# Kernel tuning notes

Measured on AMD Instinct MI355X. Metric: run time of the kernel, lower is better.

Reference implementation:

```python
import jax, jax.numpy as jnp
import numpy as np

# FP4 (e2m1) representable magnitudes: {0, 0.5, 1, 1.5, 2, 3, 4, 6}
_FP4_GRID = np.array([0.0, 0.5, 1.0, 1.5, 2.0, 3.0, 4.0, 6.0], dtype=np.float32)
_FP4_MIDS = (_FP4_GRID[1:] + _FP4_GRID[:-1]) / 2.0  # decision boundaries


def quant_fp4(x):
    """Per-tensor symmetric quantize-dequantize to FP4 e2m1 grid."""
    grid = jnp.asarray(_FP4_GRID, dtype=x.dtype)
    mids = jnp.asarray(_FP4_MIDS, dtype=x.dtype)
    scale = jnp.maximum(jnp.max(jnp.abs(x)) / 6.0, jnp.asarray(1e-12, x.dtype))
    xs = jnp.abs(x) / scale
    idx = jnp.searchsorted(mids, xs)  # nearest-grid-point index
    return jnp.sign(x) * grid[idx] * scale


def fp4_linear(x, w, b):
    # fake-quantized matmul: dequant(FP4(x)) @ dequant(FP4(w)) + b
    return jnp.matmul(quant_fp4(x), quant_fp4(w)) + b


def setup_inputs() -> dict:
    key = jax.random.key(0)
    k1, k2, k3 = jax.random.split(key, 3)
    B, D_IN, D_H, D_OUT = 4096, 4096, 16384, 4096
    x = jax.random.normal(k1, (B, D_IN), dtype=jnp.float32)
    w1 = jax.random.normal(k2, (D_IN, D_H), dtype=jnp.float32)
    b1 = jnp.zeros((D_H,), dtype=jnp.float32)
    w2 = jax.random.normal(k3, (D_H, D_OUT), dtype=jnp.float32)
    b2 = jnp.zeros((D_OUT,), dtype=jnp.float32)
    return {"x": x, "w1": w1, "b1": b1, "w2": w2, "b2": b2}


def reference(x, w1, b1, w2, b2):
    h = jax.nn.relu(fp4_linear(x, w1, b1))
    return fp4_linear(h, w2, b2)
```

## Files before the change

kernel.cpp:

```cpp
#include <hip/hip_runtime.h>
#include <hip/hip_bf16.h>


typedef float f32x4 __attribute__((ext_vector_type(4)));
typedef int   i32x4 __attribute__((ext_vector_type(4)));
typedef int   i32x8 __attribute__((ext_vector_type(8)));

#define AS1 __attribute__((address_space(1)))
#define AS3 __attribute__((address_space(3)))

__device__ __forceinline__ void wg_barrier() {
    asm volatile("" ::: "memory");
    __builtin_amdgcn_s_barrier();
    asm volatile("" ::: "memory");
}

__device__ __forceinline__ float scale_from_amax_bits(unsigned bits) {
    return fmaxf(__uint_as_float(bits) / 6.0f, 1e-12f);
}

__device__ __forceinline__ unsigned q4(float v, float inv_scale) {
    float xs = fabsf(v) * inv_scale;
    unsigned idx = 0;
    idx += (xs > 0.25f);
    idx += (xs > 0.75f);
    idx += (xs > 1.25f);
    idx += (xs > 1.75f);
    idx += (xs > 2.5f);
    idx += (xs > 3.5f);
    idx += (xs > 5.0f);
    return idx | ((v < 0.0f) ? 8u : 0u);
}

__global__ void zero4_kernel(unsigned* p) {
    if (threadIdx.x < 4) p[threadIdx.x] = 0u;
}

__global__ void sentinel_kernel(float* out, long long n) {
    long long i = (long long)blockIdx.x * blockDim.x + threadIdx.x;
    long long stride = (long long)gridDim.x * blockDim.x;
    for (; i < n; i += stride) out[i] = 1e30f;
}

__global__ void absmax3_kernel(const float* __restrict__ in0, long long n0,
                               const float* __restrict__ in1, long long n1,
                               const float* __restrict__ in2, long long n2,
                               unsigned* __restrict__ out) {
    const float* in;
    long long n;
    unsigned* o;
    long long nb, b = blockIdx.x;
    if (b < 512)       { in = in0; n = n0; o = out + 0; b -= 0;    nb = 512;  }
    else if (b < 2560) { in = in1; n = n1; o = out + 1; b -= 512;  nb = 2048; }
    else               { in = in2; n = n2; o = out + 3; b -= 2560; nb = 2048; }

    long long i = (b * blockDim.x + threadIdx.x) * 4;
    long long stride = nb * blockDim.x * 4;
    float m = 0.0f;
    for (; i < n; i += stride) {
        float4 v = *(const float4*)&in[i];
        m = fmaxf(m, fmaxf(fmaxf(fabsf(v.x), fabsf(v.y)),
                           fmaxf(fabsf(v.z), fabsf(v.w))));
    }
    #pragma unroll
    for (int off = 32; off > 0; off >>= 1)
        m = fmaxf(m, __shfl_xor(m, off));
    __shared__ float smax[4];
    int lane = threadIdx.x & 63, w = threadIdx.x >> 6;
    if (lane == 0) smax[w] = m;
    __syncthreads();
    if (threadIdx.x == 0) {
        m = fmaxf(fmaxf(smax[0], smax[1]), fmaxf(smax[2], smax[3]));
        atomicMax(o, __float_as_uint(m));
    }
}

__global__ void quant_pack_kernel(const float* __restrict__ in, long long n,
                                  const unsigned* __restrict__ amax,
                                  unsigned* __restrict__ out) {
    float inv = 1.0f / scale_from_amax_bits(*amax);
    long long i = ((long long)blockIdx.x * blockDim.x + threadIdx.x) * 8;
    long long stride = (long long)gridDim.x * blockDim.x * 8;
    for (; i < n; i += stride) {
        float4 a = *(const float4*)&in[i];
        float4 b = *(const float4*)&in[i + 4];
        unsigned u = q4(a.x, inv)        | (q4(a.y, inv) << 4)
                   | (q4(a.z, inv) << 8) | (q4(a.w, inv) << 12)
                   | (q4(b.x, inv) << 16)| (q4(b.y, inv) << 20)
                   | (q4(b.z, inv) << 24)| (q4(b.w, inv) << 28);
        out[i >> 3] = u;
    }
}

__global__ void quant_transpose_pack_kernel(const float* __restrict__ in, int R, int C,
                                            const unsigned* __restrict__ amax,
                                            unsigned char* __restrict__ out) {
    __shared__ float tile[64][65];
    float inv = 1.0f / scale_from_amax_bits(*amax);
    int t = threadIdx.x;
    int CT = C >> 6;
    int tc = blockIdx.x % CT;
    int tr = blockIdx.x / CT;
    int r0 = t >> 4;
    int c0 = (t & 15) * 4;
    #pragma unroll
    for (int it = 0; it < 4; ++it) {
        int r = r0 + it * 16;
        float4 v = *(const float4*)&in[(size_t)(tr * 64 + r) * C + tc * 64 + c0];
        tile[r][c0 + 0] = v.x;
        tile[r][c0 + 1] = v.y;
        tile[r][c0 + 2] = v.z;
        tile[r][c0 + 3] = v.w;
    }
    __syncthreads();
    int c = t >> 2;
    int rch = (t & 3) * 16;
    unsigned u0 = 0, u1 = 0;
    #pragma unroll
    for (int j = 0; j < 8; ++j) u0 |= q4(tile[rch + j][c], inv) << (4 * j);
    #pragma unroll
    for (int j = 0; j < 8; ++j) u1 |= q4(tile[rch + 8 + j][c], inv) << (4 * j);
    uint2 o; o.x = u0; o.y = u1;
    *(uint2*)&out[(size_t)(tc * 64 + c) * (R >> 1) + (size_t)(tr * 32) + (rch >> 1)] = o;
}

__device__ __forceinline__ f32x4 mm16(i32x4 a, i32x4 b, f32x4 c) {
    i32x8 a8 = {a[0], a[1], a[2], a[3], 0, 0, 0, 0};
    i32x8 b8 = {b[0], b[1], b[2], b[3], 0, 0, 0, 0};
    return __builtin_amdgcn_mfma_scale_f32_16x16x128_f8f6f4(
        a8, b8, c, 4, 4,
        0, 0x7f7f7f7f,
        0, 0x7f7f7f7f);
}

template <int RELU, int FUSE_AMAX>
__global__ __launch_bounds__(256, 2)
void gemm_fp4_a(const unsigned char* __restrict__ Ap,
                const unsigned char* __restrict__ Bp,
                float* __restrict__ C, const float* __restrict__ bias,
                const unsigned* __restrict__ amaxA,
                const unsigned* __restrict__ amaxB,
                unsigned* __restrict__ amaxOut,
                int M, int N, int K) {
    __shared__ alignas(16) unsigned char As[2][128 * 128];
    __shared__ alignas(16) unsigned char Bs[2][128 * 128];
    __shared__ float smax[4];

    int nwg = gridDim.x, cpx = nwg >> 3;
    int wg = (blockIdx.x & 7) * cpx + (blockIdx.x >> 3);
    int MT = M >> 7;
    int tm = wg % MT, tn = wg / MT;

    int tid = threadIdx.x, lane = tid & 63, wid = tid >> 6;
    int wr = wid >> 1, wc = wid & 1;

    size_t Kb = (size_t)(K >> 1);

    int cs = ((lane & 7) ^ ((lane >> 3) & 7)) << 4;
    int srow = wid * 32 + (lane >> 3);
    const unsigned char* Abase = Ap + (size_t)(tm * 128 + srow) * Kb + cs;
    const unsigned char* Bbase = Bp + (size_t)(tn * 128 + srow) * Kb + cs;
    char* AsB = (char*)As;
    char* BsB = (char*)Bs;
    int ldsOff = wid * 4096;

#define STAGE_A(d, kt)                                                        \
    do {                                                                      \
        _Pragma("unroll")                                                     \
        for (int i_ = 0; i_ < 4; ++i_) {                                      \
            __builtin_amdgcn_global_load_lds(                                 \
                (const AS1 void*)(Abase + (size_t)(kt) * 128 +                \
                                  (size_t)(i_ * 8) * Kb),                     \
                (AS3 void*)(AsB + ((d) << 14) + ldsOff + i_ * 1024),          \
                16, 0, 0);                                                    \
            __builtin_amdgcn_global_load_lds(                                 \
                (const AS1 void*)(Bbase + (size_t)(kt) * 128 +                \
                                  (size_t)(i_ * 8) * Kb),                     \
                (AS3 void*)(BsB + ((d) << 14) + ldsOff + i_ * 1024),          \
                16, 0, 0);                                                    \
        }                                                                     \
    } while (0)

    f32x4 acc[4][4] = {};
    int rrA = wr * 64 + (lane & 15);
    int rrB = wc * 64 + (lane & 15);

    int KT = K >> 8;

    STAGE_A(0, 0);

    for (int t = 0; t < KT; ++t) {
        int d = t & 1;
        if (t + 1 < KT) {
            STAGE_A(d ^ 1, t + 1);
            __builtin_amdgcn_sched_barrier(0);
            asm volatile("s_waitcnt vmcnt(8)" ::: "memory");
        } else {
            asm volatile("s_waitcnt vmcnt(0)" ::: "memory");
        }
        wg_barrier();

        const char* Aq = AsB + (d << 14);
        const char* Bq = BsB + (d << 14);
        #pragma unroll
        for (int ks = 0; ks < 2; ++ks) {
            int slotOff = ((ks * 4 + (lane >> 4)) ^ (lane & 7)) << 4;
            i32x4 a[4], b[4];
            #pragma unroll
            for (int mi = 0; mi < 4; ++mi)
                a[mi] = *(const i32x4*)(Aq + (rrA + mi * 16) * 128 + slotOff);
            #pragma unroll
            for (int ni = 0; ni < 4; ++ni)
                b[ni] = *(const i32x4*)(Bq + (rrB + ni * 16) * 128 + slotOff);
            #pragma unroll
            for (int mi = 0; mi < 4; ++mi)
                #pragma unroll
                for (int ni = 0; ni < 4; ++ni)
                    acc[mi][ni] = mm16(a[mi], b[ni], acc[mi][ni]);
        }
        asm volatile("s_waitcnt lgkmcnt(0)" ::: "memory");
        wg_barrier();
    }
#undef STAGE_A

    float s = scale_from_amax_bits(*amaxA) * scale_from_amax_bits(*amaxB);
    float vmax = 0.0f;
    int rowBase = tm * 128 + wr * 64 + (lane >> 4) * 4;
    int colBase = tn * 128 + wc * 64 + (lane & 15);
    #pragma unroll
    for (int mi = 0; mi < 4; ++mi) {
        #pragma unroll
        for (int ni = 0; ni < 4; ++ni) {
            int col = colBase + ni * 16;
            float bv = bias[col];
            int row = rowBase + mi * 16;
            #pragma unroll
            for (int r = 0; r < 4; ++r) {
                float v = acc[mi][ni][r] * s + bv;
                if (RELU) v = fmaxf(v, 0.0f);
                if (FUSE_AMAX) vmax = fmaxf(vmax, fabsf(v));
                C[(size_t)(row + r) * N + col] = v;
            }
        }
    }
    if (FUSE_AMAX) {
        #pragma unroll
        for (int off = 32; off > 0; off >>= 1)
            vmax = fmaxf(vmax, __shfl_xor(vmax, off));
        if (lane == 0) smax[wid] = vmax;
        __syncthreads();
        if (tid == 0) {
            vmax = fmaxf(fmaxf(smax[0], smax[1]), fmaxf(smax[2], smax[3]));
            atomicMax(amaxOut, __float_as_uint(vmax));
        }
    }
}

template <int RELU, int FUSE_AMAX>
__global__ __launch_bounds__(256, 4)
void gemm_fp4_b(const unsigned char* __restrict__ Ap,
                const unsigned char* __restrict__ Bp,
                float* __restrict__ C, const float* __restrict__ bias,
                const unsigned* __restrict__ amaxA,
                const unsigned* __restrict__ amaxB,
                unsigned* __restrict__ amaxOut,
                int M, int N, int K) {
    __shared__ alignas(16) unsigned char As[2][128 * 64];
    __shared__ alignas(16) unsigned char Bs[2][128 * 64];
    __shared__ float smax[4];

    int nwg = gridDim.x, cpx = nwg >> 3;
    int wg = (blockIdx.x & 7) * cpx + (blockIdx.x >> 3);
    int MT = M >> 7;
    int tm = wg % MT, tn = wg / MT;

    int tid = threadIdx.x, lane = tid & 63, wid = tid >> 6;
    int wr = wid >> 1, wc = wid & 1;

    size_t Kb = (size_t)(K >> 1);

    int csw = ((tid & 3) ^ ((tid >> 3) & 3)) << 4;
    int srow = tid >> 2;
    const unsigned char* Abase = Ap + (size_t)(tm * 128 + srow) * Kb + csw;
    const unsigned char* Bbase = Bp + (size_t)(tn * 128 + srow) * Kb + csw;
    char* AsB = (char*)As;
    char* BsB = (char*)Bs;
    int dstOff = wid << 10;

#define STAGE_B(d, kt)                                                        \
    do {                                                                      \
        _Pragma("unroll")                                                     \
        for (int i_ = 0; i_ < 2; ++i_) {                                      \
            __builtin_amdgcn_global_load_lds(                                 \
                (const AS1 void*)(Abase + (size_t)(kt) * 64 +                 \
                                  (size_t)(i_ * 64) * Kb),                    \
                (AS3 void*)(AsB + ((d) << 13) + (i_ << 12) + dstOff),         \
                16, 0, 0);                                                    \
            __builtin_amdgcn_global_load_lds(                                 \
                (const AS1 void*)(Bbase + (size_t)(kt) * 64 +                 \
                                  (size_t)(i_ * 64) * Kb),                    \
                (AS3 void*)(BsB + ((d) << 13) + (i_ << 12) + dstOff),         \
                16, 0, 0);                                                    \
        }                                                                     \
    } while (0)

    f32x4 acc[4][4] = {};
    int rrA = wr * 64 + (lane & 15);
    int rrB = wc * 64 + (lane & 15);
    int slotOff = (((lane >> 4) ^ ((lane >> 1) & 3)) << 4);

    int KT = K >> 7;

    STAGE_B(0, 0);

    for (int t = 0; t < KT; ++t) {
        int d = t & 1;
        if (t + 1 < KT) {
            STAGE_B(d ^ 1, t + 1);
            __builtin_amdgcn_sched_barrier(0);
            asm volatile("s_waitcnt vmcnt(4)" ::: "memory");
        } else {
            asm volatile("s_waitcnt vmcnt(0)" ::: "memory");
        }
        wg_barrier();

        const char* Aq = AsB + (d << 13);
        const char* Bq = BsB + (d << 13);
        i32x4 a[4], b[4];
        #pragma unroll
        for (int mi = 0; mi < 4; ++mi)
            a[mi] = *(const i32x4*)(Aq + (rrA + mi * 16) * 64 + slotOff);
        #pragma unroll
        for (int ni = 0; ni < 4; ++ni)
            b[ni] = *(const i32x4*)(Bq + (rrB + ni * 16) * 64 + slotOff);
        #pragma unroll
        for (int mi = 0; mi < 4; ++mi)
            #pragma unroll
            for (int ni = 0; ni < 4; ++ni)
                acc[mi][ni] = mm16(a[mi], b[ni], acc[mi][ni]);

        asm volatile("s_waitcnt lgkmcnt(0)" ::: "memory");
        wg_barrier();
    }
#undef STAGE_B

    float s = scale_from_amax_bits(*amaxA) * scale_from_amax_bits(*amaxB);
    float vmax = 0.0f;
    int rowBase = tm * 128 + wr * 64 + (lane >> 4) * 4;
    int colBase = tn * 128 + wc * 64 + (lane & 15);
    #pragma unroll
    for (int mi = 0; mi < 4; ++mi) {
        #pragma unroll
        for (int ni = 0; ni < 4; ++ni) {
            int col = colBase + ni * 16;
            float bv = bias[col];
            int row = rowBase + mi * 16;
            #pragma unroll
            for (int r = 0; r < 4; ++r) {
                float v = acc[mi][ni][r] * s + bv;
                if (RELU) v = fmaxf(v, 0.0f);
                if (FUSE_AMAX) vmax = fmaxf(vmax, fabsf(v));
                C[(size_t)(row + r) * N + col] = v;
            }
        }
    }
    if (FUSE_AMAX) {
        #pragma unroll
        for (int off = 32; off > 0; off >>= 1)
            vmax = fmaxf(vmax, __shfl_xor(vmax, off));
        if (lane == 0) smax[wid] = vmax;
        __syncthreads();
        if (tid == 0) {
            vmax = fmaxf(fmaxf(smax[0], smax[1]), fmaxf(smax[2], smax[3]));
            atomicMax(amaxOut, __float_as_uint(vmax));
        }
    }
}

extern "C" void kernel_launch(void* const* d_in, const int* in_sizes, int n_in,
                              void* d_out, int out_size, void* d_ws, size_t ws_size,
                              hipStream_t stream) {
    const float* x  = (const float*)d_in[0];
    const float* w1 = (const float*)d_in[1];
    const float* b1 = (const float*)d_in[2];
    const float* w2 = (const float*)d_in[3];
    const float* b2 = (const float*)d_in[4];
    float* out = (float*)d_out;

    const int B = 4096, DIN = 4096, DH = 16384, DOUT = 4096;

    const size_t off_amax = 0;
    const size_t off_Xq   = 256;
    const size_t off_W    = off_Xq + (size_t)B * DIN / 2;
    const size_t off_h    = off_W + (size_t)DIN * DH / 2;
    const size_t off_Hq   = off_h + (size_t)B * DH * 4;
    const size_t needed   = off_Hq + (size_t)B * DH / 2;

    if (ws_size < needed) {
        sentinel_kernel<<<2048, 256, 0, stream>>>(out, (long long)out_size);
        return;
    }

    char* ws = (char*)d_ws;
    unsigned* amax = (unsigned*)(ws + off_amax);
    unsigned char* Xq = (unsigned char*)(ws + off_Xq);
    unsigned char* Wq = (unsigned char*)(ws + off_W);
    float*         h  = (float*)(ws + off_h);
    unsigned char* Hq = (unsigned char*)(ws + off_Hq);

    zero4_kernel<<<1, 64, 0, stream>>>(amax);

    absmax3_kernel<<<4608, 256, 0, stream>>>(x, (long long)B * DIN,
                                             w1, (long long)DIN * DH,
                                             w2, (long long)DH * DOUT, amax);

    quant_pack_kernel<<<2048, 256, 0, stream>>>(x, (long long)B * DIN, amax + 0,
                                                (unsigned*)Xq);
    quant_transpose_pack_kernel<<<(DIN / 64) * (DH / 64), 256, 0, stream>>>(
        w1, DIN, DH, amax + 1, Wq);

    gemm_fp4_a<1, 1><<<(B / 128) * (DH / 128), 256, 0, stream>>>(
        Xq, Wq, h, b1, amax + 0, amax + 1, amax + 2, B, DH, DIN);

    quant_pack_kernel<<<2048, 256, 0, stream>>>(h, (long long)B * DH, amax + 2,
                                                (unsigned*)Hq);
    quant_transpose_pack_kernel<<<(DH / 64) * (DOUT / 64), 256, 0, stream>>>(
        w2, DH, DOUT, amax + 3, Wq);

    gemm_fp4_b<0, 0><<<(B / 128) * (DOUT / 128), 256, 0, stream>>>(
        Hq, Wq, out, b2, amax + 2, amax + 3, nullptr, B, DOUT, DH);
}
```

Measured before the change: 733.4 us.

## Split absmax per tensor, reverse quant traversal for cache reuse, simplify GEMM pipelines

Result: faster. 709.7 us (-3.2%).

```diff
diff --git a/kernel.cpp b/kernel.cpp
--- a/kernel.cpp
+++ b/kernel.cpp
@@ -8,12 +8,6 @@
 
 #define AS1 __attribute__((address_space(1)))
 #define AS3 __attribute__((address_space(3)))
-
-__device__ __forceinline__ void wg_barrier() {
-    asm volatile("" ::: "memory");
-    __builtin_amdgcn_s_barrier();
-    asm volatile("" ::: "memory");
-}
 
 __device__ __forceinline__ float scale_from_amax_bits(unsigned bits) {
     return fmaxf(__uint_as_float(bits) / 6.0f, 1e-12f);
@@ -42,20 +36,10 @@
     for (; i < n; i += stride) out[i] = 1e30f;
 }
 
-__global__ void absmax3_kernel(const float* __restrict__ in0, long long n0,
-                               const float* __restrict__ in1, long long n1,
-                               const float* __restrict__ in2, long long n2,
-                               unsigned* __restrict__ out) {
-    const float* in;
-    long long n;
-    unsigned* o;
-    long long nb, b = blockIdx.x;
-    if (b < 512)       { in = in0; n = n0; o = out + 0; b -= 0;    nb = 512;  }
-    else if (b < 2560) { in = in1; n = n1; o = out + 1; b -= 512;  nb = 2048; }
-    else               { in = in2; n = n2; o = out + 3; b -= 2560; nb = 2048; }
-
-    long long i = (b * blockDim.x + threadIdx.x) * 4;
-    long long stride = nb * blockDim.x * 4;
+__global__ void absmax_kernel(const float* __restrict__ in, long long n,
+                              unsigned* __restrict__ out) {
+    long long i = ((long long)blockIdx.x * blockDim.x + threadIdx.x) * 4;
+    long long stride = (long long)gridDim.x * blockDim.x * 4;
     float m = 0.0f;
     for (; i < n; i += stride) {
         float4 v = *(const float4*)&in[i];
@@ -71,24 +55,26 @@
     __syncthreads();
     if (threadIdx.x == 0) {
         m = fmaxf(fmaxf(smax[0], smax[1]), fmaxf(smax[2], smax[3]));
-        atomicMax(o, __float_as_uint(m));
-    }
-}
-
-__global__ void quant_pack_kernel(const float* __restrict__ in, long long n,
-                                  const unsigned* __restrict__ amax,
-                                  unsigned* __restrict__ out) {
+        atomicMax(out, __float_as_uint(m));
+    }
+}
+
+__global__ void quant_pack_rev_kernel(const float* __restrict__ in, long long n,
+                                      const unsigned* __restrict__ amax,
+                                      unsigned* __restrict__ out) {
     float inv = 1.0f / scale_from_amax_bits(*amax);
-    long long i = ((long long)blockIdx.x * blockDim.x + threadIdx.x) * 8;
-    long long stride = (long long)gridDim.x * blockDim.x * 8;
-    for (; i < n; i += stride) {
+    long long nw = n >> 3;
+    long long gid = (long long)blockIdx.x * blockDim.x + threadIdx.x;
+    long long gs = (long long)gridDim.x * blockDim.x;
+    for (long long j = nw - 1 - gid; j >= 0; j -= gs) {
+        long long i = j * 8;
         float4 a = *(const float4*)&in[i];
         float4 b = *(const float4*)&in[i + 4];
         unsigned u = q4(a.x, inv)        | (q4(a.y, inv) << 4)
                    | (q4(a.z, inv) << 8) | (q4(a.w, inv) << 12)
                    | (q4(b.x, inv) << 16)| (q4(b.y, inv) << 20)
                    | (q4(b.z, inv) << 24)| (q4(b.w, inv) << 28);
-        out[i >> 3] = u;
+        out[j] = u;
     }
 }
 
@@ -98,9 +84,10 @@
     __shared__ float tile[64][65];
     float inv = 1.0f / scale_from_amax_bits(*amax);
     int t = threadIdx.x;
+    int bid = gridDim.x - 1 - blockIdx.x;
     int CT = C >> 6;
-    int tc = blockIdx.x % CT;
-    int tr = blockIdx.x / CT;
+    int tc = bid % CT;
+    int tr = bid / CT;
     int r0 = t >> 4;
     int c0 = (t & 15) * 4;
     #pragma unroll
@@ -128,22 +115,33 @@
     i32x8 a8 = {a[0], a[1], a[2], a[3], 0, 0, 0, 0};
     i32x8 b8 = {b[0], b[1], b[2], b[3], 0, 0, 0, 0};
     return __builtin_amdgcn_mfma_scale_f32_16x16x128_f8f6f4(
-        a8, b8, c, 4, 4,
-        0, 0x7f7f7f7f,
-        0, 0x7f7f7f7f);
-}
+        a8, b8, c, 4, 4, 0, 0x7f7f7f7f, 0, 0x7f7f7f7f);
+}
+
+#define AMAX_EPILOG                                                           \
+    if (FUSE_AMAX) {                                                          \
+        _Pragma("unroll")                                                     \
+        for (int off = 32; off > 0; off >>= 1)                                \
+            vmax = fmaxf(vmax, __shfl_xor(vmax, off));                        \
+        if (lane == 0) smax[wid] = vmax;                                      \
+        __syncthreads();                                                      \
+        if (tid == 0) {                                                       \
+            vmax = fmaxf(fmaxf(smax[0], smax[1]), fmaxf(smax[2], smax[3]));   \
+            atomicMax(amaxOut, __float_as_uint(vmax));                        \
+        }                                                                     \
+    }
 
 template <int RELU, int FUSE_AMAX>
 __global__ __launch_bounds__(256, 2)
-void gemm_fp4_a(const unsigned char* __restrict__ Ap,
-                const unsigned char* __restrict__ Bp,
-                float* __restrict__ C, const float* __restrict__ bias,
-                const unsigned* __restrict__ amaxA,
-                const unsigned* __restrict__ amaxB,
-                unsigned* __restrict__ amaxOut,
-                int M, int N, int K) {
-    __shared__ alignas(16) unsigned char As[2][128 * 128];
-    __shared__ alignas(16) unsigned char Bs[2][128 * 128];
+void gemm_fp4_g1(const unsigned char* __restrict__ Ap,
+                 const unsigned char* __restrict__ Bp,
+                 float* __restrict__ C, const float* __restrict__ bias,
+                 const unsigned* __restrict__ amaxA,
+                 const unsigned* __restrict__ amaxB,
+                 unsigned* __restrict__ amaxOut,
+                 int M, int N, int K) {
+    __shared__ alignas(16) unsigned char As[128 * 128];
+    __shared__ alignas(16) unsigned char Bs[128 * 128];
     __shared__ float smax[4];
 
     int nwg = gridDim.x, cpx = nwg >> 3;
@@ -164,64 +162,41 @@
     char* BsB = (char*)Bs;
     int ldsOff = wid * 4096;
 
-#define STAGE_A(d, kt)                                                        \
-    do {                                                                      \
-        _Pragma("unroll")                                                     \
-        for (int i_ = 0; i_ < 4; ++i_) {                                      \
-            __builtin_amdgcn_global_load_lds(                                 \
-                (const AS1 void*)(Abase + (size_t)(kt) * 128 +                \
-                                  (size_t)(i_ * 8) * Kb),                     \
-                (AS3 void*)(AsB + ((d) << 14) + ldsOff + i_ * 1024),          \
-                16, 0, 0);                                                    \
-            __builtin_amdgcn_global_load_lds(                                 \
-                (const AS1 void*)(Bbase + (size_t)(kt) * 128 +                \
-                                  (size_t)(i_ * 8) * Kb),                     \
-                (AS3 void*)(BsB + ((d) << 14) + ldsOff + i_ * 1024),          \
-                16, 0, 0);                                                    \
-        }                                                                     \
-    } while (0)
-
     f32x4 acc[4][4] = {};
     int rrA = wr * 64 + (lane & 15);
     int rrB = wc * 64 + (lane & 15);
 
     int KT = K >> 8;
-
-    STAGE_A(0, 0);
-
-    for (int t = 0; t < KT; ++t) {
-        int d = t & 1;
-        if (t + 1 < KT) {
-            STAGE_A(d ^ 1, t + 1);
-            __builtin_amdgcn_sched_barrier(0);
-            asm volatile("s_waitcnt vmcnt(8)" ::: "memory");
-        } else {
-            asm volatile("s_waitcnt vmcnt(0)" ::: "memory");
+    for (int kt = 0; kt < KT; ++kt) {
+        #pragma unroll
+        for (int i = 0; i < 4; ++i) {
+            __builtin_amdgcn_global_load_lds(
+                (const AS1 void*)(Abase + (size_t)kt * 128 + (size_t)(i * 8) * Kb),
+                (AS3 void*)(AsB + ldsOff + i * 1024), 16, 0, 0);
+            __builtin_amdgcn_global_load_lds(
+                (const AS1 void*)(Bbase + (size_t)kt * 128 + (size_t)(i * 8) * Kb),
+                (AS3 void*)(BsB + ldsOff + i * 1024), 16, 0, 0);
         }
-        wg_barrier();
-
-        const char* Aq = AsB + (d << 14);
-        const char* Bq = BsB + (d << 14);
+        __syncthreads();
+
         #pragma unroll
         for (int ks = 0; ks < 2; ++ks) {
             int slotOff = ((ks * 4 + (lane >> 4)) ^ (lane & 7)) << 4;
             i32x4 a[4], b[4];
             #pragma unroll
             for (int mi = 0; mi < 4; ++mi)
-                a[mi] = *(const i32x4*)(Aq + (rrA + mi * 16) * 128 + slotOff);
+                a[mi] = *(const i32x4*)(AsB + (rrA + mi * 16) * 128 + slotOff);
             #pragma unroll
             for (int ni = 0; ni < 4; ++ni)
-                b[ni] = *(const i32x4*)(Bq + (rrB + ni * 16) * 128 + slotOff);
+                b[ni] = *(const i32x4*)(BsB + (rrB + ni * 16) * 128 + slotOff);
             #pragma unroll
             for (int mi = 0; mi < 4; ++mi)
                 #pragma unroll
                 for (int ni = 0; ni < 4; ++ni)
                     acc[mi][ni] = mm16(a[mi], b[ni], acc[mi][ni]);
         }
-        asm volatile("s_waitcnt lgkmcnt(0)" ::: "memory");
-        wg_barrier();
-    }
-#undef STAGE_A
+        __syncthreads();
+    }
 
     float s = scale_from_amax_bits(*amaxA) * scale_from_amax_bits(*amaxB);
     float vmax = 0.0f;
@@ -243,28 +218,18 @@
             }
         }
     }
-    if (FUSE_AMAX) {
-        #pragma unroll
-        for (int off = 32; off > 0; off >>= 1)
-            vmax = fmaxf(vmax, __shfl_xor(vmax, off));
-        if (lane == 0) smax[wid] = vmax;
-        __syncthreads();
-        if (tid == 0) {
-            vmax = fmaxf(fmaxf(smax[0], smax[1]), fmaxf(smax[2], smax[3]));
-            atomicMax(amaxOut, __float_as_uint(vmax));
-        }
-    }
+    AMAX_EPILOG
 }
 
 template <int RELU, int FUSE_AMAX>
-__global__ __launch_bounds__(256, 4)
-void gemm_fp4_b(const unsigned char* __restrict__ Ap,
-                const unsigned char* __restrict__ Bp,
-                float* __restrict__ C, const float* __restrict__ bias,
-                const unsigned* __restrict__ amaxA,
-                const unsigned* __restrict__ amaxB,
-                unsigned* __restrict__ amaxOut,
-                int M, int N, int K) {
+__global__ __launch_bounds__(256, 2)
+void gemm_fp4_g2(const unsigned char* __restrict__ Ap,
+                 const unsigned char* __restrict__ Bp,
+                 float* __restrict__ C, const float* __restrict__ bias,
+                 const unsigned* __restrict__ amaxA,
+                 const unsigned* __restrict__ amaxB,
+                 unsigned* __restrict__ amaxOut,
+                 int M, int N, int K) {
     __shared__ alignas(16) unsigned char As[2][128 * 64];
     __shared__ alignas(16) unsigned char Bs[2][128 * 64];
     __shared__ float smax[4];
@@ -287,7 +252,7 @@
     char* BsB = (char*)Bs;
     int dstOff = wid << 10;
 
-#define STAGE_B(d, kt)                                                        \
+#define STAGE_G2(d, kt)                                                       \
     do {                                                                      \
         _Pragma("unroll")                                                     \
         for (int i_ = 0; i_ < 2; ++i_) {                                      \
@@ -310,19 +275,13 @@
     int slotOff = (((lane >> 4) ^ ((lane >> 1) & 3)) << 4);
 
     int KT = K >> 7;
-
-    STAGE_B(0, 0);
+    STAGE_G2(0, 0);
+    __syncthreads();
 
     for (int t = 0; t < KT; ++t) {
         int d = t & 1;
-        if (t + 1 < KT) {
-            STAGE_B(d ^ 1, t + 1);
-            __builtin_amdgcn_sched_barrier(0);
-            asm volatile("s_waitcnt vmcnt(4)" ::: "memory");
-        } else {
-            asm volatile("s_waitcnt vmcnt(0)" ::: "memory");
-        }
-        wg_barrier();
+        if (t + 1 < KT) STAGE_G2(d ^ 1, t + 1);
+        __builtin_amdgcn_sched_barrier(0);
 
         const char* Aq = AsB + (d << 13);
         const char* Bq = BsB + (d << 13);
@@ -338,11 +297,9 @@
             #pragma unroll
             for (int ni = 0; ni < 4; ++ni)
                 acc[mi][ni] = mm16(a[mi], b[ni], acc[mi][ni]);
-
-        asm volatile("s_waitcnt lgkmcnt(0)" ::: "memory");
-        wg_barrier();
-    }
-#undef STAGE_B
+        __syncthreads();
+    }
+#undef STAGE_G2
 
     float s = scale_from_amax_bits(*amaxA) * scale_from_amax_bits(*amaxB);
     float vmax = 0.0f;
@@ -364,17 +321,7 @@
             }
         }
     }
-    if (FUSE_AMAX) {
-        #pragma unroll
-        for (int off = 32; off > 0; off >>= 1)
-            vmax = fmaxf(vmax, __shfl_xor(vmax, off));
-        if (lane == 0) smax[wid] = vmax;
-        __syncthreads();
-        if (tid == 0) {
-            vmax = fmaxf(fmaxf(smax[0], smax[1]), fmaxf(smax[2], smax[3]));
-            atomicMax(amaxOut, __float_as_uint(vmax));
-        }
-    }
+    AMAX_EPILOG
 }
 
 extern "C" void kernel_launch(void* const* d_in, const int* in_sizes, int n_in,
@@ -410,23 +357,24 @@
 
     zero4_kernel<<<1, 64, 0, stream>>>(amax);
 
-    absmax3_kernel<<<4608, 256, 0, stream>>>(x, (long long)B * DIN,
-                                             w1, (long long)DIN * DH,
-                                             w2, (long long)DH * DOUT, amax);
-
-    quant_pack_kernel<<<2048, 256, 0, stream>>>(x, (long long)B * DIN, amax + 0,
-                                                (unsigned*)Xq);
+    absmax_kernel<<<2048, 256, 0, stream>>>(w1, (long long)DIN * DH, amax + 1);
     quant_transpose_pack_kernel<<<(DIN / 64) * (DH / 64), 256, 0, stream>>>(
         w1, DIN, DH, amax + 1, Wq);
 
-    gemm_fp4_a<1, 1><<<(B / 128) * (DH / 128), 256, 0, stream>>>(
+    absmax_kernel<<<2048, 256, 0, stream>>>(x, (long long)B * DIN, amax + 0);
+    quant_pack_rev_kernel<<<2048, 256, 0, stream>>>(x, (long long)B * DIN,
+                                                    amax + 0, (unsigned*)Xq);
+
+    gemm_fp4_g1<1, 1><<<(B / 128) * (DH / 128), 256, 0, stream>>>(
         Xq, Wq, h, b1, amax + 0, amax + 1, amax + 2, B, DH, DIN);
 
-    quant_pack_kernel<<<2048, 256, 0, stream>>>(h, (long long)B * DH, amax + 2,
-                                                (unsigned*)Hq);
+    quant_pack_rev_kernel<<<2048, 256, 0, stream>>>(h, (long long)B * DH,
+                                                    amax + 2, (unsigned*)Hq);
+
+    absmax_kernel<<<2048, 256, 0, stream>>>(w2, (long long)DH * DOUT, amax + 3);
     quant_transpose_pack_kernel<<<(DH / 64) * (DOUT / 64), 256, 0, stream>>>(
         w2, DH, DOUT, amax + 3, Wq);
 
-    gemm_fp4_b<0, 0><<<(B / 128) * (DOUT / 128), 256, 0, stream>>>(
+    gemm_fp4_g2<0, 0><<<(B / 128) * (DOUT / 128), 256, 0, stream>>>(
         Hq, Wq, out, b2, amax + 2, amax + 3, nullptr, B, DOUT, DH);
 }
```
